# Optimization experiments

Hardware: AMD Instinct MI355X
Metric: run time of the kernel (lower is better)

The kernel has to match this reference:

```python
import jax, jax.numpy as jnp
import numpy as np

EDGE_R = 7                      # box-filter radius -> 15x15 all-ones kernel
EBT_BALANCE = (1.0, 0.8, 0.5)   # Edge / Boundary-band / Texture balance
LAYER_WEIGHT = 1.0              # single (non-list) prediction path


def setup_inputs() -> dict:
    key = jax.random.key(0)
    k1, k2 = jax.random.split(key)
    b, c, h, w = 16, 1, 1024, 1024
    # Pred are probabilities (module applies BCELoss directly); keep away from {0,1}
    Pred = jax.random.uniform(k1, (b, c, h, w), jnp.float32, 0.01, 0.99)
    label = jax.random.randint(k2, (b, c, h, w), 0, 2).astype(jnp.int32)
    return {"Pred": Pred, "label": label}


def _ebt_loss(Pred, label_f):
    b, c, h, w = label_f.shape
    num_total = float(b * c * h * w)
    mask = jnp.clip(label_f, 0.0, 1.0)
    k = 2 * EDGE_R + 1
    filt = jnp.ones((1, 1, k, k), mask.dtype)
    # 15x15 all-ones box filter with 'same' padding (edge dilation of the mask)
    edge = jax.lax.conv_general_dilated(
        mask, filt, window_strides=(1, 1),
        padding=[(EDGE_R, EDGE_R), (EDGE_R, EDGE_R)],
        dimension_numbers=("NCHW", "OIHW", "NCHW"))
    edge = jnp.where(edge > 0, 1.0, 0.0)  # binarize (conv output is >= 0)
    B = edge - label_f           # boundary band around foreground
    T = 1.0 - edge               # texture (far-from-edge background)
    num_E = mask.sum()
    num_B = B.sum()
    num_T = T.sum()
    weight = ((1.0 - num_E / num_total) * EBT_BALANCE[0] * mask
              + (1.0 - num_B / num_total) * EBT_BALANCE[1] * B
              + (1.0 - num_T / num_total) * EBT_BALANCE[2] * T)
    # BCELoss(reduction='none'): -(t*log(p) + (1-t)*log(1-p))
    bce = -(label_f * jnp.log(Pred) + (1.0 - label_f) * jnp.log1p(-Pred))
    return (weight * bce).mean()


def reference(Pred, label):
    label_f = label.astype(jnp.float32)
    return LAYER_WEIGHT * _ebt_loss(Pred, label_f)
```

## Files before the change

### kernel.cpp

```cpp
#include <hip/hip_runtime.h>
#include <math.h>

#define IMG_H 1024
#define IMG_W 1024
#define NB    16
#define NROWS (NB * IMG_H)
#define WPR   (IMG_W / 32)
#define NTOTAL 16777216.0
#define NBUCKET 1024

struct Acc {
    double sE, sB, sT;
    unsigned int cMask, cEdge;
};

__global__ void k_dilate_h(const int* __restrict__ label,
                           unsigned int* __restrict__ maskbits,
                           unsigned int* __restrict__ rowor) {
    __shared__ unsigned int lm[256];
    const int t = threadIdx.x;
    const int wave = t >> 6, lane = t & 63;
    const long rowBase = (long)blockIdx.x * 8;
    const long pixBase = rowBase * IMG_W;

    #pragma unroll 4
    for (int it = 0; it < 32; ++it) {
        int idx = it * 256 + t;
        int lab = label[pixBase + idx];
        unsigned long long bal = __ballot(lab != 0);
        if (lane == 0) {
            int wi = (it * 256 + wave * 64) >> 5;
            lm[wi]     = (unsigned int)bal;
            lm[wi + 1] = (unsigned int)(bal >> 32);
        }
    }
    __syncthreads();

    const int wd = t & 31;
    unsigned int prev = wd        ? lm[t - 1] : 0u;
    unsigned int cur  =             lm[t];
    unsigned int next = (wd < 31) ? lm[t + 1] : 0u;
    unsigned long long Wn = (((unsigned long long)prev) >> 16)
                          | (((unsigned long long)cur)  << 16)
                          | (((unsigned long long)next) << 48);
    unsigned long long acc = Wn;
    #pragma unroll
    for (int d = 1; d <= 7; ++d) acc |= (Wn >> d) | (Wn << d);

    long o = rowBase * WPR + t;
    maskbits[o] = cur;
    rowor[o]    = (unsigned int)(acc >> 16);
}

__global__ void k_bce(const float* __restrict__ pred,
                      const unsigned int* __restrict__ maskbits,
                      const unsigned int* __restrict__ rowor,
                      Acc* __restrict__ acc) {
    __shared__ unsigned int eM[32], eE[32];
    __shared__ float redf[12];
    __shared__ unsigned int redc[8];

    const int t  = threadIdx.x;
    const int Rf = blockIdx.x;
    const int b  = Rf >> 10;
    const int i  = Rf & 1023;

    if (t < 32) { eE[t] = 0u; eM[t] = maskbits[(long)Rf * WPR + t]; }
    __syncthreads();

    if (t < 128) {
        const int w = t & 31, g = t >> 5;
        int lo = i - 7; if (lo < 0) lo = 0;
        int hi = i + 7; if (hi > 1023) hi = 1023;
        unsigned int e = 0u;
        const unsigned int* base = rowor + ((long)b << 10) * WPR + w;
        for (int ri = lo + g; ri <= hi; ri += 4) e |= base[(long)ri * WPR];
        atomicOr(&eE[w], e);
    }
    __syncthreads();

    float sE = 0.f, sB = 0.f, sT = 0.f;
    unsigned int cM = 0, cE = 0;
    const float4 pv = ((const float4*)(pred + (long)Rf * IMG_W))[t];
    const unsigned int sh = (t & 7) << 2;
    const unsigned int mN = (eM[t >> 3] >> sh) & 0xFu;
    const unsigned int eN = (eE[t >> 3] >> sh) & 0xFu;
    const float pj[4] = {pv.x, pv.y, pv.z, pv.w};
    #pragma unroll
    for (int j = 0; j < 4; ++j) {
        unsigned int m = (mN >> j) & 1u;
        unsigned int e = (eN >> j) & 1u;
        float bce = m ? -__logf(pj[j]) : -__logf(1.0f - pj[j]);
        sE += m ? bce : 0.f;
        sB += (e & ~m & 1u) ? bce : 0.f;
        sT += e ? 0.f : bce;
        cM += m;  cE += e;
    }

    #pragma unroll
    for (int off = 32; off; off >>= 1) {
        sE += __shfl_down(sE, off);
        sB += __shfl_down(sB, off);
        sT += __shfl_down(sT, off);
        cM += __shfl_down(cM, off);
        cE += __shfl_down(cE, off);
    }
    const int wave = t >> 6, lane = t & 63;
    if (lane == 0) {
        redf[wave * 3 + 0] = sE;
        redf[wave * 3 + 1] = sB;
        redf[wave * 3 + 2] = sT;
        redc[wave * 2 + 0] = cM;
        redc[wave * 2 + 1] = cE;
    }
    __syncthreads();
    if (t == 0) {
        float tE = 0.f, tB = 0.f, tT = 0.f;
        unsigned int tM = 0, tEd = 0;
        #pragma unroll
        for (int wv = 0; wv < 4; ++wv) {
            tE += redf[wv * 3 + 0];
            tB += redf[wv * 3 + 1];
            tT += redf[wv * 3 + 2];
            tM  += redc[wv * 2 + 0];
            tEd += redc[wv * 2 + 1];
        }
        Acc* a = &acc[Rf & (NBUCKET - 1)];
        atomicAdd(&a->sE, (double)tE);
        atomicAdd(&a->sB, (double)tB);
        atomicAdd(&a->sT, (double)tT);
        atomicAdd(&a->cMask, tM);
        atomicAdd(&a->cEdge, tEd);
    }
}

__global__ void k_final(const Acc* __restrict__ acc, float* __restrict__ out) {
    __shared__ double redd[12];
    __shared__ double redn[8];
    const int t = threadIdx.x;
    double sE = 0.0, sB = 0.0, sT = 0.0, nM = 0.0, nEd = 0.0;
    for (int idx = t; idx < NBUCKET; idx += 256) {
        sE += acc[idx].sE;  sB += acc[idx].sB;  sT += acc[idx].sT;
        nM += (double)acc[idx].cMask;  nEd += (double)acc[idx].cEdge;
    }
    #pragma unroll
    for (int off = 32; off; off >>= 1) {
        sE += __shfl_down(sE, off);
        sB += __shfl_down(sB, off);
        sT += __shfl_down(sT, off);
        nM += __shfl_down(nM, off);
        nEd += __shfl_down(nEd, off);
    }
    const int wave = t >> 6, lane = t & 63;
    if (lane == 0) {
        redd[wave * 3 + 0] = sE;
        redd[wave * 3 + 1] = sB;
        redd[wave * 3 + 2] = sT;
        redn[wave * 2 + 0] = nM;
        redn[wave * 2 + 1] = nEd;
    }
    __syncthreads();
    if (t == 0) {
        double tE = 0, tB = 0, tT = 0, tM = 0, tEd = 0;
        #pragma unroll
        for (int wv = 0; wv < 4; ++wv) {
            tE += redd[wv * 3 + 0];
            tB += redd[wv * 3 + 1];
            tT += redd[wv * 3 + 2];
            tM  += redn[wv * 2 + 0];
            tEd += redn[wv * 2 + 1];
        }
        double nBnd = tEd - tM;
        double nT   = NTOTAL - tEd;
        double wE = (1.0 - tM   / NTOTAL) * 1.0;
        double wB = (1.0 - nBnd / NTOTAL) * 0.8;
        double wT = (1.0 - nT   / NTOTAL) * 0.5;
        out[0] = (float)((wE * tE + wB * tB + wT * tT) / NTOTAL);
    }
}

extern "C" void kernel_launch(void* const* d_in, const int* in_sizes, int n_in,
                              void* d_out, int out_size, void* d_ws, size_t ws_size,
                              hipStream_t stream) {
    const float* pred  = (const float*)d_in[0];
    const int*   label = (const int*)d_in[1];
    float* out = (float*)d_out;

    char* ws = (char*)d_ws;
    Acc* acc = (Acc*)ws;
    unsigned int* maskbits = (unsigned int*)(ws + (size_t)NBUCKET * sizeof(Acc));
    unsigned int* rowor    = (unsigned int*)(ws + (size_t)NBUCKET * sizeof(Acc)
                                               + (size_t)NROWS * WPR * 4);

    hipMemsetAsync(acc, 0, (size_t)NBUCKET * sizeof(Acc), stream);
    k_dilate_h<<<NROWS / 8, 256, 0, stream>>>(label, maskbits, rowor);
    k_bce<<<NROWS, 256, 0, stream>>>(pred, maskbits, rowor, acc);
    k_final<<<1, 256, 0, stream>>>(acc, out);
}
```

Before: 174.0 us.

## Process eight rows per BCE block and reformulate sums with log2 algebra

The BCE kernel now handles 8 rows per block instead of one, so each block launches 8x fewer times and does 8x fewer atomics. Each thread computes one word of the vertical edge OR for its row directly, with no shared-memory atomicOr, and counts bits with popc. Per-pixel work becomes a single log2 with three masked sums (all, edge, mask), and the boundary and texture sums are recovered algebraically in the final kernel. The risks are a longer serial vertical OR loop per thread (15 loads) and small float-precision differences from subtracting partial sums.

Measured after the change: 162.0 us. 1.07x faster.

```diff
diff --git a/kernel.cpp b/kernel.cpp
--- a/kernel.cpp
+++ b/kernel.cpp
@@ -8,9 +8,10 @@
 #define WPR   (IMG_W / 32)
 #define NTOTAL 16777216.0
 #define NBUCKET 1024
+#define LN2 0.6931471805599453
 
 struct Acc {
-    double sE, sB, sT;
+    double s2A, s2E, s2M;
     unsigned int cMask, cEdge;
 };
 
@@ -56,79 +57,84 @@
                       const unsigned int* __restrict__ maskbits,
                       const unsigned int* __restrict__ rowor,
                       Acc* __restrict__ acc) {
-    __shared__ unsigned int eM[32], eE[32];
+    __shared__ unsigned int eM[256], eE[256];
     __shared__ float redf[12];
     __shared__ unsigned int redc[8];
 
     const int t  = threadIdx.x;
-    const int Rf = blockIdx.x;
-    const int b  = Rf >> 10;
-    const int i  = Rf & 1023;
-
-    if (t < 32) { eE[t] = 0u; eM[t] = maskbits[(long)Rf * WPR + t]; }
-    __syncthreads();
-
-    if (t < 128) {
-        const int w = t & 31, g = t >> 5;
+    const int R0 = blockIdx.x * 8;
+    const int b  = R0 >> 10;
+    const int i0 = R0 & 1023;
+
+    const int g = t >> 5, w = t & 31;
+    {
+        const int i = i0 + g;
         int lo = i - 7; if (lo < 0) lo = 0;
         int hi = i + 7; if (hi > 1023) hi = 1023;
+        const unsigned int* base = rowor + ((long)b << 10) * WPR + w;
         unsigned int e = 0u;
-        const unsigned int* base = rowor + ((long)b << 10) * WPR + w;
-        for (int ri = lo + g; ri <= hi; ri += 4) e |= base[(long)ri * WPR];
-        atomicOr(&eE[w], e);
-    }
-    __syncthreads();
-
-    float sE = 0.f, sB = 0.f, sT = 0.f;
-    unsigned int cM = 0, cE = 0;
-    const float4 pv = ((const float4*)(pred + (long)Rf * IMG_W))[t];
-    const unsigned int sh = (t & 7) << 2;
-    const unsigned int mN = (eM[t >> 3] >> sh) & 0xFu;
-    const unsigned int eN = (eE[t >> 3] >> sh) & 0xFu;
-    const float pj[4] = {pv.x, pv.y, pv.z, pv.w};
-    #pragma unroll
-    for (int j = 0; j < 4; ++j) {
-        unsigned int m = (mN >> j) & 1u;
-        unsigned int e = (eN >> j) & 1u;
-        float bce = m ? -__logf(pj[j]) : -__logf(1.0f - pj[j]);
-        sE += m ? bce : 0.f;
-        sB += (e & ~m & 1u) ? bce : 0.f;
-        sT += e ? 0.f : bce;
-        cM += m;  cE += e;
+        for (int ri = lo; ri <= hi; ++ri) e |= base[(long)ri * WPR];
+        eE[t] = e;
+        unsigned int m = maskbits[(long)(R0 + g) * WPR + w];
+        eM[t] = m;
+    }
+    unsigned int cM = __popc(eM[t]), cE = __popc(eE[t]);
+    __syncthreads();
+
+    float s2A = 0.f, s2E = 0.f, s2M = 0.f;
+    const float4* p4 = (const float4*)(pred + (long)R0 * IMG_W);
+    #pragma unroll
+    for (int k = 0; k < 8; ++k) {
+        const int f = t + k * 256;
+        const float4 pv = p4[f];
+        const unsigned int sh = (f & 7) << 2;
+        const unsigned int mN = (eM[f >> 3] >> sh) & 0xFu;
+        const unsigned int eN = (eE[f >> 3] >> sh) & 0xFu;
+        const float pj[4] = {pv.x, pv.y, pv.z, pv.w};
+        #pragma unroll
+        for (int j = 0; j < 4; ++j) {
+            const unsigned int m = (mN >> j) & 1u;
+            const unsigned int e = (eN >> j) & 1u;
+            const float x = m ? pj[j] : 1.0f - pj[j];
+            const float l = __log2f(x);
+            s2A += l;
+            s2E += e ? l : 0.f;
+            s2M += m ? l : 0.f;
+        }
     }
 
     #pragma unroll
     for (int off = 32; off; off >>= 1) {
-        sE += __shfl_down(sE, off);
-        sB += __shfl_down(sB, off);
-        sT += __shfl_down(sT, off);
-        cM += __shfl_down(cM, off);
-        cE += __shfl_down(cE, off);
+        s2A += __shfl_down(s2A, off);
+        s2E += __shfl_down(s2E, off);
+        s2M += __shfl_down(s2M, off);
+        cM  += __shfl_down(cM, off);
+        cE  += __shfl_down(cE, off);
     }
     const int wave = t >> 6, lane = t & 63;
     if (lane == 0) {
-        redf[wave * 3 + 0] = sE;
-        redf[wave * 3 + 1] = sB;
-        redf[wave * 3 + 2] = sT;
+        redf[wave * 3 + 0] = s2A;
+        redf[wave * 3 + 1] = s2E;
+        redf[wave * 3 + 2] = s2M;
         redc[wave * 2 + 0] = cM;
         redc[wave * 2 + 1] = cE;
     }
     __syncthreads();
     if (t == 0) {
-        float tE = 0.f, tB = 0.f, tT = 0.f;
+        float tA = 0.f, tEg = 0.f, tMg = 0.f;
         unsigned int tM = 0, tEd = 0;
         #pragma unroll
         for (int wv = 0; wv < 4; ++wv) {
-            tE += redf[wv * 3 + 0];
-            tB += redf[wv * 3 + 1];
-            tT += redf[wv * 3 + 2];
+            tA  += redf[wv * 3 + 0];
+            tEg += redf[wv * 3 + 1];
+            tMg += redf[wv * 3 + 2];
             tM  += redc[wv * 2 + 0];
             tEd += redc[wv * 2 + 1];
         }
-        Acc* a = &acc[Rf & (NBUCKET - 1)];
-        atomicAdd(&a->sE, (double)tE);
-        atomicAdd(&a->sB, (double)tB);
-        atomicAdd(&a->sT, (double)tT);
+        Acc* a = &acc[blockIdx.x & (NBUCKET - 1)];
+        atomicAdd(&a->s2A, (double)tA);
+        atomicAdd(&a->s2E, (double)tEg);
+        atomicAdd(&a->s2M, (double)tMg);
         atomicAdd(&a->cMask, tM);
         atomicAdd(&a->cEdge, tEd);
     }
@@ -138,44 +144,49 @@
     __shared__ double redd[12];
     __shared__ double redn[8];
     const int t = threadIdx.x;
-    double sE = 0.0, sB = 0.0, sT = 0.0, nM = 0.0, nEd = 0.0;
+    double sA = 0.0, sEg = 0.0, sMg = 0.0, nM = 0.0, nEd = 0.0;
     for (int idx = t; idx < NBUCKET; idx += 256) {
-        sE += acc[idx].sE;  sB += acc[idx].sB;  sT += acc[idx].sT;
-        nM += (double)acc[idx].cMask;  nEd += (double)acc[idx].cEdge;
+        sA  += acc[idx].s2A;  sEg += acc[idx].s2E;  sMg += acc[idx].s2M;
+        nM  += (double)acc[idx].cMask;  nEd += (double)acc[idx].cEdge;
     }
     #pragma unroll
     for (int off = 32; off; off >>= 1) {
-        sE += __shfl_down(sE, off);
-        sB += __shfl_down(sB, off);
-        sT += __shfl_down(sT, off);
-        nM += __shfl_down(nM, off);
+        sA  += __shfl_down(sA, off);
+        sEg += __shfl_down(sEg, off);
+        sMg += __shfl_down(sMg, off);
+        nM  += __shfl_down(nM, off);
         nEd += __shfl_down(nEd, off);
     }
     const int wave = t >> 6, lane = t & 63;
     if (lane == 0) {
-        redd[wave * 3 + 0] = sE;
-        redd[wave * 3 + 1] = sB;
-        redd[wave * 3 + 2] = sT;
+        redd[wave * 3 + 0] = sA;
+        redd[wave * 3 + 1] = sEg;
+        redd[wave * 3 + 2] = sMg;
         redn[wave * 2 + 0] = nM;
         redn[wave * 2 + 1] = nEd;
     }
     __syncthreads();
     if (t == 0) {
-        double tE = 0, tB = 0, tT = 0, tM = 0, tEd = 0;
+        double tA = 0, tEg = 0, tMg = 0, tM = 0, tEd = 0;
         #pragma unroll
         for (int wv = 0; wv < 4; ++wv) {
-            tE += redd[wv * 3 + 0];
-            tB += redd[wv * 3 + 1];
-            tT += redd[wv * 3 + 2];
+            tA  += redd[wv * 3 + 0];
+            tEg += redd[wv * 3 + 1];
+            tMg += redd[wv * 3 + 2];
             tM  += redn[wv * 2 + 0];
             tEd += redn[wv * 2 + 1];
         }
+        double sE_bce = -LN2 * tMg;
+        double sEdge  = -LN2 * tEg;
+        double sAll   = -LN2 * tA;
+        double sB_bce = sEdge - sE_bce;
+        double sT_bce = sAll - sEdge;
         double nBnd = tEd - tM;
         double nT   = NTOTAL - tEd;
         double wE = (1.0 - tM   / NTOTAL) * 1.0;
         double wB = (1.0 - nBnd / NTOTAL) * 0.8;
         double wT = (1.0 - nT   / NTOTAL) * 0.5;
-        out[0] = (float)((wE * tE + wB * tB + wT * tT) / NTOTAL);
+        out[0] = (float)((wE * sE_bce + wB * sB_bce + wT * sT_bce) / NTOTAL);
     }
 }
 
@@ -194,6 +205,6 @@
 
     hipMemsetAsync(acc, 0, (size_t)NBUCKET * sizeof(Acc), stream);
     k_dilate_h<<<NROWS / 8, 256, 0, stream>>>(label, maskbits, rowor);
-    k_bce<<<NROWS, 256, 0, stream>>>(pred, maskbits, rowor, acc);
+    k_bce<<<NROWS / 8, 256, 0, stream>>>(pred, maskbits, rowor, acc);
     k_final<<<1, 256, 0, stream>>>(acc, out);
 }
```
